# Performance work log

Hardware: AMD Instinct MI355X
Metric: run time of the kernel (lower is better)

Reference implementation:

```python
import jax, jax.numpy as jnp
import numpy as np

N_NODES = 100000
N_EDGES = 1600000


def _graph_conv(num_nodes, edge_index, feat, w, b, in_feats, out_feats):
    src, dst = edge_index[0], edge_index[1]
    # degree of source endpoints, clamp(min=1)^-0.5
    deg = jax.ops.segment_sum(jnp.ones_like(src, dtype=jnp.float32), src, num_segments=num_nodes)
    norm = jnp.power(jnp.clip(deg, 1.0), -0.5)[:, None]  # [N,1]
    feat = feat * norm
    if in_feats > out_feats:
        feat = feat @ w                                   # [N,out]
        rst = jax.ops.segment_sum(feat[src], dst, num_segments=num_nodes)
    else:
        rst = jax.ops.segment_sum(feat[src], dst, num_segments=num_nodes)
        rst = rst @ w
    rst = rst * norm + b
    return jax.nn.relu(rst)


def setup_inputs() -> dict:
    key = jax.random.key(0)
    ks = jax.random.split(key, 8)
    features = jax.random.normal(ks[0], (N_NODES, 256), dtype=jnp.float32)
    e_subgraph = jax.random.randint(ks[1], (2, N_EDGES), 0, N_NODES, dtype=jnp.int64 if jax.config.jax_enable_x64 else jnp.int32)
    n_subgraph = jnp.zeros((N_NODES,), dtype=jnp.int32)
    to_fetch = jax.random.randint(ks[2], (16,), 0, N_NODES, dtype=jnp.int32)
    # GraphConv weights (xavier-like scale), Linear weight (out,in) per F.linear
    w1 = jax.random.normal(ks[3], (256, 128), dtype=jnp.float32) * (2.0 / (256 + 128)) ** 0.5
    b1 = jnp.zeros((128,), dtype=jnp.float32)
    w2 = jax.random.normal(ks[4], (128, 128), dtype=jnp.float32) * (2.0 / (128 + 128)) ** 0.5
    b2 = jnp.zeros((128,), dtype=jnp.float32)
    w3 = jax.random.normal(ks[5], (16, 128), dtype=jnp.float32) * (2.0 / 128) ** 0.5
    b3 = jnp.zeros((16,), dtype=jnp.float32)
    return {"n_subgraph": n_subgraph, "e_subgraph": e_subgraph, "to_fetch": to_fetch,
            "features": features, "w1": w1, "b1": b1, "w2": w2, "b2": b2, "w3": w3, "b3": b3}


def reference(n_subgraph, e_subgraph, to_fetch, features, w1, b1, w2, b2, w3, b3):
    num_nodes = n_subgraph.shape[0]
    h = features.astype(jnp.float32)
    h = _graph_conv(num_nodes, e_subgraph, h, w1, b1, 256, 128)
    h = _graph_conv(num_nodes, e_subgraph, h, w2, b2, 128, 128)
    h = h @ w3.T + b3  # F.linear
    return (h, h)
```

## Files before the change

### kernel.cpp

```cpp
#include <hip/hip_runtime.h>

#define AP 40
#define H2P 136
#define PB 120
#define NPB 256
#define NBUKMAX 512
#define CAPE 8192

typedef short bf16x8 __attribute__((ext_vector_type(8)));
typedef float f32x4 __attribute__((ext_vector_type(4)));

static __device__ __forceinline__ ushort f2bf(float f) {
  unsigned u = __float_as_uint(f);
  unsigned r = (u + 0x7fffu + ((u >> 16) & 1u)) >> 16;
  return (ushort)r;
}
static __device__ __forceinline__ float bflo(unsigned u) { return __uint_as_float(u << 16); }
static __device__ __forceinline__ float bfhi(unsigned u) { return __uint_as_float(u & 0xffff0000u); }
static __device__ __forceinline__ unsigned packbf(float lo, float hi) {
  return (unsigned)f2bf(lo) | ((unsigned)f2bf(hi) << 16);
}

__global__ __launch_bounds__(256) void k_hist2(const int* __restrict__ src,
                                               const int* __restrict__ dst, int E,
                                               unsigned* __restrict__ planes, int HW,
                                               int* __restrict__ hist) {
  __shared__ unsigned lds[25600];
  __shared__ int cnt[NBUKMAX];
  const int per = (E + PB - 1) / PB;
  const int s0 = blockIdx.x * per;
  const int s1 = min(E, s0 + per);
  for (int i = threadIdx.x; i < HW; i += 256) lds[i] = 0u;
  for (int i = threadIdx.x; i < NBUKMAX; i += 256) cnt[i] = 0;
  __syncthreads();
  for (int j = s0 + threadIdx.x; j < s1; j += 256) {
    int k = src[j];
    atomicAdd(&lds[k >> 2], 1u << ((k & 3) * 8));
    atomicAdd(&cnt[dst[j] >> 8], 1);
  }
  __syncthreads();
  unsigned* out = planes + (size_t)blockIdx.x * HW;
  for (int i = threadIdx.x; i < HW; i += 256) __builtin_nontemporal_store(lds[i], &out[i]);
  for (int i = threadIdx.x; i < NBUKMAX; i += 256) hist[i * PB + blockIdx.x] = cnt[i];
}

__global__ void k_reduce_cvt(const unsigned* __restrict__ planes, int HW,
                             float* __restrict__ nrm, int N, int nrb,
                             const float* __restrict__ w1, const float* __restrict__ w2,
                             const float* __restrict__ w3, ushort* __restrict__ w1T,
                             ushort* __restrict__ w2T, ushort* __restrict__ w3b) {
  if ((int)blockIdx.x < nrb) {
    int w = blockIdx.x * 256 + threadIdx.x;
    if (w >= HW) return;
    const unsigned* base = planes + w;
    unsigned c0 = 0, c1 = 0, c2 = 0, c3 = 0;
    for (int b = 0; b < PB; b++) {
      unsigned u = __builtin_nontemporal_load(&base[(size_t)b * HW]);
      c0 += u & 255u; c1 += (u >> 8) & 255u; c2 += (u >> 16) & 255u; c3 += u >> 24;
    }
    int n0 = w * 4;
    unsigned c[4] = {c0, c1, c2, c3};
#pragma unroll
    for (int j = 0; j < 4; j++)
      if (n0 + j < N) {
        float d = (float)c[j];
        if (d < 1.f) d = 1.f;
        nrm[n0 + j] = 1.f / sqrtf(d);
      }
  } else {
    int i = (blockIdx.x - nrb) * 256 + threadIdx.x;
    if (i < 32768) {
      int c = i >> 8, k = i & 255;
      w1T[i] = f2bf(w1[k * 128 + c]);
    } else if (i < 49152) {
      int j = i - 32768;
      int c = j >> 7, k = j & 127;
      w2T[j] = f2bf(w2[k * 128 + c]);
    } else if (i < 51200) {
      int j = i - 49152;
      w3b[j] = f2bf(w3[j]);
    }
  }
}

__global__ __launch_bounds__(NBUKMAX) void k_p0_scan(int* __restrict__ hist) {
  __shared__ int s[NBUKMAX];
  int b = threadIdx.x;
  const int bi = b * PB;
  int tot = 0;
  for (int blk = 0; blk < PB; blk++) tot += hist[bi + blk];
  s[b] = tot;
  __syncthreads();
  for (int o = 1; o < NBUKMAX; o <<= 1) {
    int x = (b >= o) ? s[b - o] : 0;
    __syncthreads();
    s[b] += x;
    __syncthreads();
  }
  int base = s[b] - tot;
  for (int blk = 0; blk < PB; blk++) {
    int t = hist[bi + blk];
    hist[bi + blk] = base;
    base += t;
  }
}

__global__ __launch_bounds__(256) void k_p1_scatter(const int* __restrict__ src,
                                                    const int* __restrict__ dst, int E,
                                                    const int* __restrict__ hist,
                                                    unsigned* __restrict__ pairs) {
  __shared__ int cur[NBUKMAX];
  for (int i = threadIdx.x; i < NBUKMAX; i += 256) cur[i] = hist[i * PB + blockIdx.x];
  __syncthreads();
  const int per = (E + PB - 1) / PB;
  const int s0 = blockIdx.x * per;
  const int s1 = min(E, s0 + per);
  for (int j = s0 + threadIdx.x; j < s1; j += 256) {
    int d = dst[j];
    int pos = atomicAdd(&cur[d >> 8], 1);
    pairs[pos] = ((unsigned)src[j] << 8) | (unsigned)(d & 255);
  }
}

__global__ __launch_bounds__(256) void k_p2_place(const unsigned* __restrict__ pairs,
                                                  const int* __restrict__ hist,
                                                  int* __restrict__ csr,
                                                  int* __restrict__ row_start,
                                                  int N, int E) {
  __shared__ int stage[CAPE];
  __shared__ int cnt[NPB];
  __shared__ int scn[NPB];
  const int b = blockIdx.x;
  const int t = threadIdx.x;
  const int n0 = b << 8;
  const int n1 = min(N, n0 + NPB);
  const int nn = n1 - n0;
  const int e0 = hist[b * PB];
  const int e1 = hist[(b + 1) * PB];
  for (int i = t; i < nn; i += 256) cnt[i] = 0;
  __syncthreads();
  for (int j = e0 + t; j < e1; j += 256) atomicAdd(&cnt[pairs[j] & 255u], 1);
  __syncthreads();
  int v = (t < nn) ? cnt[t] : 0;
  scn[t] = v;
  __syncthreads();
  for (int o = 1; o < NPB; o <<= 1) {
    int x = (t >= o) ? scn[t - o] : 0;
    __syncthreads();
    scn[t] += x;
    __syncthreads();
  }
  int excl = scn[t] - v;
  if (t < nn) row_start[n0 + t] = e0 + excl;
  if (t == NPB - 1 && n1 == N) row_start[N] = e0 + scn[t];
  __syncthreads();
  if (t < nn) cnt[t] = excl;
  __syncthreads();
  const int seg = e1 - e0;
  if (seg <= CAPE) {
    for (int j = e0 + t; j < e1; j += 256) {
      unsigned pr = pairs[j];
      int rpos = atomicAdd(&cnt[pr & 255u], 1);
      stage[rpos] = (int)(pr >> 8);
    }
    __syncthreads();
    for (int j = t; j < seg; j += 256) csr[e0 + j] = stage[j];
  } else {
    for (int j = e0 + t; j < e1; j += 256) {
      unsigned pr = pairs[j];
      int rpos = atomicAdd(&cnt[pr & 255u], 1);
      csr[e0 + rpos] = (int)(pr >> 8);
    }
  }
}

__global__ __launch_bounds__(256) void k_gemm1_mfma(const float* __restrict__ feat,
                                                    const ushort* __restrict__ w1T,
                                                    const float* __restrict__ nrm,
                                                    ushort* __restrict__ Xb, int N) {
  __shared__ ushort As[128 * AP];
  __shared__ ushort Bs[128 * AP];
  const int tid = threadIdx.x;
  const int row0 = blockIdx.x * 128;
  const int wv = tid >> 6, lane = tid & 63;
  const int rbase = wv * 32;
  const int lr = lane & 15;
  const int kl = (lane >> 4) * 8;

  f32x4 acc[8][2];
#pragma unroll
  for (int ni = 0; ni < 8; ni++)
#pragma unroll
    for (int mi = 0; mi < 2; mi++) acc[ni][mi] = (f32x4)0.f;

  for (int k0 = 0; k0 < 256; k0 += 32) {
    __syncthreads();
#pragma unroll
    for (int j = 0; j < 4; j++) {
      int e = (tid + j * 256) * 4;
      int r = e >> 5, k = e & 31;
      int gr = row0 + r;
      float4 v = make_float4(0.f, 0.f, 0.f, 0.f);
      if (gr < N) v = *(const float4*)&feat[(size_t)gr * 256 + k0 + k];
      ushort4 u;
      u.x = f2bf(v.x); u.y = f2bf(v.y); u.z = f2bf(v.z); u.w = f2bf(v.w);
      *(ushort4*)&As[r * AP + k] = u;
    }
#pragma unroll
    for (int j = 0; j < 4; j++) {
      int e = (tid + j * 256) * 4;
      int c = e >> 5, k = e & 31;
      ushort4 v = *(const ushort4*)&w1T[(size_t)c * 256 + k0 + k];
      *(ushort4*)&Bs[c * AP + k] = v;
    }
    __syncthreads();
    bf16x8 bfrag[2], afrag[8];
#pragma unroll
    for (int mi = 0; mi < 2; mi++)
      bfrag[mi] = *(const bf16x8*)&As[(rbase + mi * 16 + lr) * AP + kl];
#pragma unroll
    for (int ni = 0; ni < 8; ni++)
      afrag[ni] = *(const bf16x8*)&Bs[(ni * 16 + lr) * AP + kl];
#pragma unroll
    for (int ni = 0; ni < 8; ni++)
#pragma unroll
      for (int mi = 0; mi < 2; mi++)
        acc[ni][mi] = __builtin_amdgcn_mfma_f32_16x16x32_bf16(afrag[ni], bfrag[mi], acc[ni][mi], 0, 0, 0);
  }
#pragma unroll
  for (int mi = 0; mi < 2; mi++) {
    int gr = row0 + rbase + mi * 16 + lr;
    if (gr < N) {
      float nv = nrm[gr];
#pragma unroll
      for (int ni = 0; ni < 8; ni++) {
        int c0 = ni * 16 + (lane >> 4) * 4;
        ushort4 u;
        u.x = f2bf(acc[ni][mi][0] * nv);
        u.y = f2bf(acc[ni][mi][1] * nv);
        u.z = f2bf(acc[ni][mi][2] * nv);
        u.w = f2bf(acc[ni][mi][3] * nv);
        *(ushort4*)&Xb[(size_t)gr * 128 + c0] = u;
      }
    }
  }
}

__global__ __launch_bounds__(256) void k_agg_bf(const ushort* __restrict__ Xin,
                                                const int* __restrict__ rs,
                                                const int* __restrict__ csr,
                                                const float* __restrict__ nrm,
                                                const float* __restrict__ bias,
                                                ushort* __restrict__ Out, int N, int fused) {
  const int wv = threadIdx.x >> 6, lane = threadIdx.x & 63;
  const int d = blockIdx.x * 4 + wv;
  if (d >= N) return;
  const unsigned* X = (const unsigned*)Xin;
  int s0 = rs[d], s1 = rs[d + 1];
  float a0 = 0.f, a1 = 0.f;
  int j = s0;
  for (; j + 8 <= s1; j += 8) {
    int idx[8];
#pragma unroll
    for (int q = 0; q < 8; q++) idx[q] = csr[j + q];
    unsigned u[8];
#pragma unroll
    for (int q = 0; q < 8; q++) u[q] = X[(size_t)idx[q] * 64 + lane];
#pragma unroll
    for (int q = 0; q < 8; q++) { a0 += bflo(u[q]); a1 += bfhi(u[q]); }
  }
  for (; j < s1; j++) {
    unsigned u = X[(size_t)csr[j] * 64 + lane];
    a0 += bflo(u);
    a1 += bfhi(u);
  }
  unsigned o;
  if (fused) {
    float nv = nrm[d];
    float2 b = *(const float2*)&bias[lane * 2];
    float h0 = fmaxf(a0 * nv + b.x, 0.f) * nv;
    float h1 = fmaxf(a1 * nv + b.y, 0.f) * nv;
    o = packbf(h0, h1);
  } else {
    o = packbf(a0, a1);
  }
  __builtin_nontemporal_store(o, &((unsigned*)Out)[(size_t)d * 64 + lane]);
}

__global__ __launch_bounds__(256) void k_gemm23_mfma(const ushort* __restrict__ Agg2,
                                                     const float* __restrict__ nrm,
                                                     const ushort* __restrict__ w2T,
                                                     const float* __restrict__ b2,
                                                     const ushort* __restrict__ w3b,
                                                     const float* __restrict__ b3,
                                                     float* __restrict__ out, int N) {
  __shared__ __align__(16) char lds_raw[128 * H2P * 2];
  ushort* As = (ushort*)lds_raw;
  ushort* Bs = As + 128 * AP;
  ushort* h2s = (ushort*)lds_raw;

  const int tid = threadIdx.x;
  const int row0 = blockIdx.x * 128;
  const int wv = tid >> 6, lane = tid & 63;
  const int rbase = wv * 32;
  const int lr = lane & 15;
  const int kl = (lane >> 4) * 8;

  f32x4 acc[8][2];
#pragma unroll
  for (int ni = 0; ni < 8; ni++)
#pragma unroll
    for (int mi = 0; mi < 2; mi++) acc[ni][mi] = (f32x4)0.f;

  for (int k0 = 0; k0 < 128; k0 += 32) {
    __syncthreads();
#pragma unroll
    for (int j = 0; j < 4; j++) {
      int e = (tid + j * 256) * 4;
      int r = e >> 5, k = e & 31;
      int gr = row0 + r;
      ushort4 v = make_ushort4(0, 0, 0, 0);
      if (gr < N) v = *(const ushort4*)&Agg2[(size_t)gr * 128 + k0 + k];
      *(ushort4*)&As[r * AP + k] = v;
    }
#pragma unroll
    for (int j = 0; j < 4; j++) {
      int e = (tid + j * 256) * 4;
      int c = e >> 5, k = e & 31;
      ushort4 v = *(const ushort4*)&w2T[(size_t)c * 128 + k0 + k];
      *(ushort4*)&Bs[c * AP + k] = v;
    }
    __syncthreads();
    bf16x8 bfrag[2], afrag[8];
#pragma unroll
    for (int mi = 0; mi < 2; mi++)
      bfrag[mi] = *(const bf16x8*)&As[(rbase + mi * 16 + lr) * AP + kl];
#pragma unroll
    for (int ni = 0; ni < 8; ni++)
      afrag[ni] = *(const bf16x8*)&Bs[(ni * 16 + lr) * AP + kl];
#pragma unroll
    for (int ni = 0; ni < 8; ni++)
#pragma unroll
      for (int mi = 0; mi < 2; mi++)
        acc[ni][mi] = __builtin_amdgcn_mfma_f32_16x16x32_bf16(afrag[ni], bfrag[mi], acc[ni][mi], 0, 0, 0);
  }
  __syncthreads();

#pragma unroll
  for (int mi = 0; mi < 2; mi++) {
    int r = rbase + mi * 16 + lr;
    int gr = row0 + r;
    float nv = (gr < N) ? nrm[gr] : 0.f;
#pragma unroll
    for (int ni = 0; ni < 8; ni++) {
      int c0 = ni * 16 + (lane >> 4) * 4;
      float4 bb = *(const float4*)&b2[c0];
      ushort4 u;
      u.x = f2bf(fmaxf(acc[ni][mi][0] * nv + bb.x, 0.f));
      u.y = f2bf(fmaxf(acc[ni][mi][1] * nv + bb.y, 0.f));
      u.z = f2bf(fmaxf(acc[ni][mi][2] * nv + bb.z, 0.f));
      u.w = f2bf(fmaxf(acc[ni][mi][3] * nv + bb.w, 0.f));
      *(ushort4*)&h2s[r * H2P + c0] = u;
    }
  }
  f32x4 acc3[2];
  acc3[0] = (f32x4)0.f;
  acc3[1] = (f32x4)0.f;
#pragma unroll
  for (int ks = 0; ks < 4; ks++) {
    bf16x8 a3 = *(const bf16x8*)&w3b[(size_t)lr * 128 + ks * 32 + kl];
#pragma unroll
    for (int mi = 0; mi < 2; mi++) {
      bf16x8 b3f = *(const bf16x8*)&h2s[(rbase + mi * 16 + lr) * H2P + ks * 32 + kl];
      acc3[mi] = __builtin_amdgcn_mfma_f32_16x16x32_bf16(a3, b3f, acc3[mi], 0, 0, 0);
    }
  }
#pragma unroll
  for (int mi = 0; mi < 2; mi++) {
    int gr = row0 + rbase + mi * 16 + lr;
    if (gr < N) {
      int o0 = (lane >> 4) * 4;
      float4 bb = *(const float4*)&b3[o0];
      float4 v;
      v.x = acc3[mi][0] + bb.x;
      v.y = acc3[mi][1] + bb.y;
      v.z = acc3[mi][2] + bb.z;
      v.w = acc3[mi][3] + bb.w;
      *(float4*)&out[(size_t)gr * 16 + o0] = v;
      *(float4*)&out[(size_t)(N + gr) * 16 + o0] = v;
    }
  }
}

extern "C" void kernel_launch(void* const* d_in, const int* in_sizes, int n_in,
                              void* d_out, int out_size, void* d_ws, size_t ws_size,
                              hipStream_t stream) {
  const int N = in_sizes[0];
  const int E = in_sizes[1] / 2;
  const int HW = (N + 3) / 4;
  const int NBUK = (N + NPB - 1) / NPB;
  const int nrb = (HW + 255) / 256;

  const int* e_sub = (const int*)d_in[1];
  const int* src = e_sub;
  const int* dst = e_sub + E;
  const float* feat = (const float*)d_in[3];
  const float* w1 = (const float*)d_in[4];
  const float* b1 = (const float*)d_in[5];
  const float* w2 = (const float*)d_in[6];
  const float* b2 = (const float*)d_in[7];
  const float* w3 = (const float*)d_in[8];
  const float* b3 = (const float*)d_in[9];
  float* out = (float*)d_out;

  char* p = (char*)d_ws;
  auto alloc = [&](size_t bytes) { void* r = (void*)p; p += (bytes + 255) & ~(size_t)255; return r; };
  int* row_start = (int*)alloc((size_t)(N + 1) * 4);
  int* csr = (int*)alloc((size_t)E * 4);
  int* hist = (int*)alloc((size_t)(NBUKMAX + 1) * PB * 4);
  unsigned* pairs = (unsigned*)alloc((size_t)E * 4);
  float* nrm = (float*)alloc((size_t)N * 4);
  ushort* w1T = (ushort*)alloc((size_t)128 * 256 * 2);
  ushort* w2T = (ushort*)alloc((size_t)128 * 128 * 2);
  ushort* w3b = (ushort*)alloc((size_t)16 * 128 * 2);
  ushort* Xb = (ushort*)alloc((size_t)N * 128 * 2);
  ushort* Hb = (ushort*)alloc((size_t)N * 128 * 2);
  unsigned* planes = (unsigned*)alloc((size_t)PB * HW * 4);

  k_hist2<<<PB, 256, 0, stream>>>(src, dst, E, planes, HW, hist);
  k_reduce_cvt<<<nrb + 200, 256, 0, stream>>>(planes, HW, nrm, N, nrb, w1, w2, w3, w1T, w2T, w3b);
  k_p0_scan<<<1, NBUKMAX, 0, stream>>>(hist);
  k_p1_scatter<<<PB, 256, 0, stream>>>(src, dst, E, hist, pairs);
  k_p2_place<<<NBUK, 256, 0, stream>>>(pairs, hist, csr, row_start, N, E);
  k_gemm1_mfma<<<(N + 127) / 128, 256, 0, stream>>>(feat, w1T, nrm, Xb, N);
  k_agg_bf<<<(N + 3) / 4, 256, 0, stream>>>(Xb, row_start, csr, nrm, b1, Hb, N, 1);
  k_agg_bf<<<(N + 3) / 4, 256, 0, stream>>>(Hb, row_start, csr, nrm, b1, Xb, N, 0);
  k_gemm23_mfma<<<(N + 127) / 128, 256, 0, stream>>>(Xb, nrm, w2T, b2, w3b, b3, out, N);
}
```

Baseline: 323.7 us.

## Fuse bucket scan into reduce kernel and co-launch scatter with GEMM1

The single-block prefix scan now runs as an extra block of the reduce/convert kernel, with 256 threads each handling two buckets. The edge-scatter pass and the first MFMA GEMM share one launch, so the two independent phases run concurrently and two launches disappear. GEMM1 now reads weight fragments straight from global memory instead of staging them in LDS. The aggregation loop is unrolled by 4 instead of 8, and the nontemporal load/store hints are dropped. The risks are the unsynchronized scan block in the reduce kernel, heavier global weight traffic in GEMM1, and less memory-level parallelism in the gather loop.

Result: faster. 306.2 us (-5.4%).

```diff
diff --git a/kernel.cpp b/kernel.cpp
--- a/kernel.cpp
+++ b/kernel.cpp
@@ -40,7 +40,7 @@
   }
   __syncthreads();
   unsigned* out = planes + (size_t)blockIdx.x * HW;
-  for (int i = threadIdx.x; i < HW; i += 256) __builtin_nontemporal_store(lds[i], &out[i]);
+  for (int i = threadIdx.x; i < HW; i += 256) out[i] = lds[i];
   for (int i = threadIdx.x; i < NBUKMAX; i += 256) hist[i * PB + blockIdx.x] = cnt[i];
 }
 
@@ -48,14 +48,16 @@
                              float* __restrict__ nrm, int N, int nrb,
                              const float* __restrict__ w1, const float* __restrict__ w2,
                              const float* __restrict__ w3, ushort* __restrict__ w1T,
-                             ushort* __restrict__ w2T, ushort* __restrict__ w3b) {
+                             ushort* __restrict__ w2T, ushort* __restrict__ w3b,
+                             int* __restrict__ hist) {
+  __shared__ int s[256];
   if ((int)blockIdx.x < nrb) {
     int w = blockIdx.x * 256 + threadIdx.x;
     if (w >= HW) return;
     const unsigned* base = planes + w;
     unsigned c0 = 0, c1 = 0, c2 = 0, c3 = 0;
     for (int b = 0; b < PB; b++) {
-      unsigned u = __builtin_nontemporal_load(&base[(size_t)b * HW]);
+      unsigned u = base[(size_t)b * HW];
       c0 += u & 255u; c1 += (u >> 8) & 255u; c2 += (u >> 16) & 255u; c3 += u >> 24;
     }
     int n0 = w * 4;
@@ -67,7 +69,7 @@
         if (d < 1.f) d = 1.f;
         nrm[n0 + j] = 1.f / sqrtf(d);
       }
-  } else {
+  } else if ((int)blockIdx.x < nrb + 200) {
     int i = (blockIdx.x - nrb) * 256 + threadIdx.x;
     if (i < 32768) {
       int c = i >> 8, k = i & 255;
@@ -80,45 +82,107 @@
       int j = i - 49152;
       w3b[j] = f2bf(w3[j]);
     }
-  }
-}
-
-__global__ __launch_bounds__(NBUKMAX) void k_p0_scan(int* __restrict__ hist) {
-  __shared__ int s[NBUKMAX];
-  int b = threadIdx.x;
-  const int bi = b * PB;
-  int tot = 0;
-  for (int blk = 0; blk < PB; blk++) tot += hist[bi + blk];
-  s[b] = tot;
-  __syncthreads();
-  for (int o = 1; o < NBUKMAX; o <<= 1) {
-    int x = (b >= o) ? s[b - o] : 0;
-    __syncthreads();
-    s[b] += x;
-    __syncthreads();
-  }
-  int base = s[b] - tot;
-  for (int blk = 0; blk < PB; blk++) {
-    int t = hist[bi + blk];
-    hist[bi + blk] = base;
-    base += t;
-  }
-}
-
-__global__ __launch_bounds__(256) void k_p1_scatter(const int* __restrict__ src,
-                                                    const int* __restrict__ dst, int E,
-                                                    const int* __restrict__ hist,
-                                                    unsigned* __restrict__ pairs) {
+  } else {
+    int t = threadIdx.x;
+    int b0 = t * 2, b1 = t * 2 + 1;
+    int tot0 = 0, tot1 = 0;
+    for (int blk = 0; blk < PB; blk++) tot0 += hist[b0 * PB + blk];
+    for (int blk = 0; blk < PB; blk++) tot1 += hist[b1 * PB + blk];
+    int pair = tot0 + tot1;
+    s[t] = pair;
+    __syncthreads();
+    for (int o = 1; o < 256; o <<= 1) {
+      int x = (t >= o) ? s[t - o] : 0;
+      __syncthreads();
+      s[t] += x;
+      __syncthreads();
+    }
+    int base0 = s[t] - pair;
+    int base = base0;
+    for (int blk = 0; blk < PB; blk++) { int v = hist[b0 * PB + blk]; hist[b0 * PB + blk] = base; base += v; }
+    for (int blk = 0; blk < PB; blk++) { int v = hist[b1 * PB + blk]; hist[b1 * PB + blk] = base; base += v; }
+  }
+}
+
+__global__ __launch_bounds__(256) void k_p1_gemm1(const int* __restrict__ src,
+                                                  const int* __restrict__ dst, int E,
+                                                  const int* __restrict__ hist,
+                                                  unsigned* __restrict__ pairs,
+                                                  const float* __restrict__ feat,
+                                                  const ushort* __restrict__ w1T,
+                                                  const float* __restrict__ nrm,
+                                                  ushort* __restrict__ Xb, int N) {
   __shared__ int cur[NBUKMAX];
-  for (int i = threadIdx.x; i < NBUKMAX; i += 256) cur[i] = hist[i * PB + blockIdx.x];
-  __syncthreads();
-  const int per = (E + PB - 1) / PB;
-  const int s0 = blockIdx.x * per;
-  const int s1 = min(E, s0 + per);
-  for (int j = s0 + threadIdx.x; j < s1; j += 256) {
-    int d = dst[j];
-    int pos = atomicAdd(&cur[d >> 8], 1);
-    pairs[pos] = ((unsigned)src[j] << 8) | (unsigned)(d & 255);
+  __shared__ ushort As[128 * AP];
+  if ((int)blockIdx.x < PB) {
+    for (int i = threadIdx.x; i < NBUKMAX; i += 256) cur[i] = hist[i * PB + blockIdx.x];
+    __syncthreads();
+    const int per = (E + PB - 1) / PB;
+    const int s0 = blockIdx.x * per;
+    const int s1 = min(E, s0 + per);
+    for (int j = s0 + threadIdx.x; j < s1; j += 256) {
+      int d = dst[j];
+      int pos = atomicAdd(&cur[d >> 8], 1);
+      pairs[pos] = ((unsigned)src[j] << 8) | (unsigned)(d & 255);
+    }
+    return;
+  }
+  const int tid = threadIdx.x;
+  const int row0 = (blockIdx.x - PB) * 128;
+  const int wv = tid >> 6, lane = tid & 63;
+  const int rbase = wv * 32;
+  const int lr = lane & 15;
+  const int kl = (lane >> 4) * 8;
+
+  f32x4 acc[8][2];
+#pragma unroll
+  for (int ni = 0; ni < 8; ni++)
+#pragma unroll
+    for (int mi = 0; mi < 2; mi++) acc[ni][mi] = (f32x4)0.f;
+
+  for (int k0 = 0; k0 < 256; k0 += 32) {
+    __syncthreads();
+#pragma unroll
+    for (int j = 0; j < 4; j++) {
+      int e = (tid + j * 256) * 4;
+      int r = e >> 5, k = e & 31;
+      int gr = row0 + r;
+      float4 v = make_float4(0.f, 0.f, 0.f, 0.f);
+      if (gr < N) v = *(const float4*)&feat[(size_t)gr * 256 + k0 + k];
+      ushort4 u;
+      u.x = f2bf(v.x); u.y = f2bf(v.y); u.z = f2bf(v.z); u.w = f2bf(v.w);
+      *(ushort4*)&As[r * AP + k] = u;
+    }
+    __syncthreads();
+    bf16x8 bfrag[2], afrag[8];
+#pragma unroll
+    for (int mi = 0; mi < 2; mi++)
+      bfrag[mi] = *(const bf16x8*)&As[(rbase + mi * 16 + lr) * AP + kl];
+#pragma unroll
+    for (int ni = 0; ni < 8; ni++)
+      afrag[ni] = *(const bf16x8*)&w1T[(size_t)(ni * 16 + lr) * 256 + k0 + kl];
+#pragma unroll
+    for (int ni = 0; ni < 8; ni++)
+#pragma unroll
+      for (int mi = 0; mi < 2; mi++)
+        acc[ni][mi] = __builtin_amdgcn_mfma_f32_16x16x32_bf16(afrag[ni], bfrag[mi], acc[ni][mi], 0, 0, 0);
+  }
+#pragma unroll
+  for (int mi = 0; mi < 2; mi++) {
+    int gr = row0 + rbase + mi * 16 + lr;
+    if (gr < N) {
+      float nv = nrm[gr];
+#pragma unroll
+      for (int ni = 0; ni < 8; ni++) {
+        int c0 = ni * 16 + (lane >> 4) * 4;
+        ushort4 u;
+        u.x = f2bf(acc[ni][mi][0] * nv);
+        u.y = f2bf(acc[ni][mi][1] * nv);
+        u.z = f2bf(acc[ni][mi][2] * nv);
+        u.w = f2bf(acc[ni][mi][3] * nv);
+        *(ushort4*)&Xb[(size_t)gr * 128 + c0] = u;
+      }
+    }
   }
 }
 
@@ -174,78 +238,6 @@
   }
 }
 
-__global__ __launch_bounds__(256) void k_gemm1_mfma(const float* __restrict__ feat,
-                                                    const ushort* __restrict__ w1T,
-                                                    const float* __restrict__ nrm,
-                                                    ushort* __restrict__ Xb, int N) {
-  __shared__ ushort As[128 * AP];
-  __shared__ ushort Bs[128 * AP];
-  const int tid = threadIdx.x;
-  const int row0 = blockIdx.x * 128;
-  const int wv = tid >> 6, lane = tid & 63;
-  const int rbase = wv * 32;
-  const int lr = lane & 15;
-  const int kl = (lane >> 4) * 8;
-
-  f32x4 acc[8][2];
-#pragma unroll
-  for (int ni = 0; ni < 8; ni++)
-#pragma unroll
-    for (int mi = 0; mi < 2; mi++) acc[ni][mi] = (f32x4)0.f;
-
-  for (int k0 = 0; k0 < 256; k0 += 32) {
-    __syncthreads();
-#pragma unroll
-    for (int j = 0; j < 4; j++) {
-      int e = (tid + j * 256) * 4;
-      int r = e >> 5, k = e & 31;
-      int gr = row0 + r;
-      float4 v = make_float4(0.f, 0.f, 0.f, 0.f);
-      if (gr < N) v = *(const float4*)&feat[(size_t)gr * 256 + k0 + k];
-      ushort4 u;
-      u.x = f2bf(v.x); u.y = f2bf(v.y); u.z = f2bf(v.z); u.w = f2bf(v.w);
-      *(ushort4*)&As[r * AP + k] = u;
-    }
-#pragma unroll
-    for (int j = 0; j < 4; j++) {
-      int e = (tid + j * 256) * 4;
-      int c = e >> 5, k = e & 31;
-      ushort4 v = *(const ushort4*)&w1T[(size_t)c * 256 + k0 + k];
-      *(ushort4*)&Bs[c * AP + k] = v;
-    }
-    __syncthreads();
-    bf16x8 bfrag[2], afrag[8];
-#pragma unroll
-    for (int mi = 0; mi < 2; mi++)
-      bfrag[mi] = *(const bf16x8*)&As[(rbase + mi * 16 + lr) * AP + kl];
-#pragma unroll
-    for (int ni = 0; ni < 8; ni++)
-      afrag[ni] = *(const bf16x8*)&Bs[(ni * 16 + lr) * AP + kl];
-#pragma unroll
-    for (int ni = 0; ni < 8; ni++)
-#pragma unroll
-      for (int mi = 0; mi < 2; mi++)
-        acc[ni][mi] = __builtin_amdgcn_mfma_f32_16x16x32_bf16(afrag[ni], bfrag[mi], acc[ni][mi], 0, 0, 0);
-  }
-#pragma unroll
-  for (int mi = 0; mi < 2; mi++) {
-    int gr = row0 + rbase + mi * 16 + lr;
-    if (gr < N) {
-      float nv = nrm[gr];
-#pragma unroll
-      for (int ni = 0; ni < 8; ni++) {
-        int c0 = ni * 16 + (lane >> 4) * 4;
-        ushort4 u;
-        u.x = f2bf(acc[ni][mi][0] * nv);
-        u.y = f2bf(acc[ni][mi][1] * nv);
-        u.z = f2bf(acc[ni][mi][2] * nv);
-        u.w = f2bf(acc[ni][mi][3] * nv);
-        *(ushort4*)&Xb[(size_t)gr * 128 + c0] = u;
-      }
-    }
-  }
-}
-
 __global__ __launch_bounds__(256) void k_agg_bf(const ushort* __restrict__ Xin,
                                                 const int* __restrict__ rs,
                                                 const int* __restrict__ csr,
@@ -259,15 +251,14 @@
   int s0 = rs[d], s1 = rs[d + 1];
   float a0 = 0.f, a1 = 0.f;
   int j = s0;
-  for (; j + 8 <= s1; j += 8) {
-    int idx[8];
-#pragma unroll
-    for (int q = 0; q < 8; q++) idx[q] = csr[j + q];
-    unsigned u[8];
-#pragma unroll
-    for (int q = 0; q < 8; q++) u[q] = X[(size_t)idx[q] * 64 + lane];
-#pragma unroll
-    for (int q = 0; q < 8; q++) { a0 += bflo(u[q]); a1 += bfhi(u[q]); }
+  for (; j + 4 <= s1; j += 4) {
+    int i0 = csr[j], i1 = csr[j + 1], i2 = csr[j + 2], i3 = csr[j + 3];
+    unsigned u0 = X[(size_t)i0 * 64 + lane];
+    unsigned u1 = X[(size_t)i1 * 64 + lane];
+    unsigned u2 = X[(size_t)i2 * 64 + lane];
+    unsigned u3 = X[(size_t)i3 * 64 + lane];
+    a0 += (bflo(u0) + bflo(u1)) + (bflo(u2) + bflo(u3));
+    a1 += (bfhi(u0) + bfhi(u1)) + (bfhi(u2) + bfhi(u3));
   }
   for (; j < s1; j++) {
     unsigned u = X[(size_t)csr[j] * 64 + lane];
@@ -284,7 +275,7 @@
   } else {
     o = packbf(a0, a1);
   }
-  __builtin_nontemporal_store(o, &((unsigned*)Out)[(size_t)d * 64 + lane]);
+  ((unsigned*)Out)[(size_t)d * 64 + lane] = o;
 }
 
 __global__ __launch_bounds__(256) void k_gemm23_mfma(const ushort* __restrict__ Agg2,
@@ -428,11 +419,11 @@
   unsigned* planes = (unsigned*)alloc((size_t)PB * HW * 4);
 
   k_hist2<<<PB, 256, 0, stream>>>(src, dst, E, planes, HW, hist);
-  k_reduce_cvt<<<nrb + 200, 256, 0, stream>>>(planes, HW, nrm, N, nrb, w1, w2, w3, w1T, w2T, w3b);
-  k_p0_scan<<<1, NBUKMAX, 0, stream>>>(hist);
-  k_p1_scatter<<<PB, 256, 0, stream>>>(src, dst, E, hist, pairs);
+  k_reduce_cvt<<<nrb + 201, 256, 0, stream>>>(planes, HW, nrm, N, nrb, w1, w2, w3, w1T, w2T,
+                                              w3b, hist);
+  k_p1_gemm1<<<PB + (N + 127) / 128, 256, 0, stream>>>(src, dst, E, hist, pairs, feat, w1T,
+                                                       nrm, Xb, N);
   k_p2_place<<<NBUK, 256, 0, stream>>>(pairs, hist, csr, row_start, N, E);
-  k_gemm1_mfma<<<(N + 127) / 128, 256, 0, stream>>>(feat, w1T, nrm, Xb, N);
   k_agg_bf<<<(N + 3) / 4, 256, 0, stream>>>(Xb, row_start, csr, nrm, b1, Hb, N, 1);
   k_agg_bf<<<(N + 3) / 4, 256, 0, stream>>>(Hb, row_start, csr, nrm, b1, Xb, N, 0);
   k_gemm23_mfma<<<(N + 127) / 128, 256, 0, stream>>>(Xb, nrm, w2T, b2, w3b, b3, out, N);
```
